# Performance work log

Measured on AMD Instinct MI355X. Metric: run time of the kernel, lower is better.

## Reference

```python
import jax, jax.numpy as jnp
import numpy as np

N = 100_000   # nodes
E = 1_600_000 # edges
F = 128       # node_feature_dim
H = 128       # hidden_dim
A = 32        # action_dim
G = 64        # graphs in batch


def setup_inputs() -> dict:
    key = jax.random.key(0)
    ks = jax.random.split(key, 12)
    s = 0.05
    return {
        "x": jax.random.normal(ks[0], (N, F), jnp.float32),
        "edge_index": jax.random.randint(ks[1], (2, E), 0, N, dtype=jnp.int32),
        "batch": jnp.sort(jax.random.randint(ks[2], (N,), 0, G, dtype=jnp.int32)),
        "W1": jax.random.normal(ks[3], (F, H), jnp.float32) * s,
        "b1": jnp.zeros((H,), jnp.float32),
        "W2": jax.random.normal(ks[4], (H, H), jnp.float32) * s,
        "b2": jnp.zeros((H,), jnp.float32),
        "Wa": jax.random.normal(ks[5], (H, A), jnp.float32) * s,
        "ba": jnp.zeros((A,), jnp.float32),
        "Wv": jax.random.normal(ks[6], (H, 1), jnp.float32) * s,
        "bv": jnp.zeros((1,), jnp.float32),
        "log_std": jnp.zeros((A,), jnp.float32),
    }


def reference(x, edge_index, batch, W1, b1, W2, b2, Wa, ba, Wv, bv, log_std):
    src, dst = edge_index[0], edge_index[1]
    # GCN symmetric norm with self-loops: deg_i = 1 + #incoming edges
    deg = jax.ops.segment_sum(jnp.ones((E,), x.dtype), dst, num_segments=N) + 1.0
    dinv = deg ** -0.5  # [N]

    def gcn(h, W, b):
        h = h @ W                                   # [N,H] dense transform first (as PyG GCNConv)
        msg = h[src] * dinv[src, None]              # gather + src norm
        agg = jax.ops.segment_sum(msg, dst, num_segments=N) * dinv[:, None]
        agg = agg + h * (dinv * dinv)[:, None]      # self-loop contribution
        return agg + b

    h = jax.nn.relu(gcn(x, W1, b1))
    h = jax.nn.relu(gcn(h, W2, b2))

    # global_mean_pool over graph segments
    counts = jax.ops.segment_sum(jnp.ones((N,), h.dtype), batch, num_segments=G)
    pooled = jax.ops.segment_sum(h, batch, num_segments=G) / jnp.maximum(counts, 1.0)[:, None]

    action_mean = pooled @ Wa + ba                  # [G,A]
    value = (pooled @ Wv + bv)[:, 0]                # [G]
    return action_mean, jnp.exp(log_std), value
```

## Files before the change

kernel.cpp:

```cpp
#include <hip/hip_runtime.h>
#include <hip/hip_bf16.h>

#define FDIM 128
#define HDIM 128
#define ADIM 32
#define PCH 128
#define BSH 6
#define BWD 64
#define CHUNK 8192
#define MAXNB 2048

#define CP(p) ((((p) & 7) << 4) | ((p) >> 3))

typedef short v8s __attribute__((ext_vector_type(8)));
typedef float v4f __attribute__((ext_vector_type(4)));
typedef float v2f __attribute__((ext_vector_type(2)));

static __device__ __forceinline__ float bflo(unsigned int u) {
    return __builtin_bit_cast(float, u << 16);
}
static __device__ __forceinline__ float bfhi(unsigned int u) {
    return __builtin_bit_cast(float, u & 0xffff0000u);
}
static __device__ __forceinline__ unsigned int bfpack(float a, float b) {
    unsigned int ua = __builtin_bit_cast(unsigned int, a);
    unsigned int ub = __builtin_bit_cast(unsigned int, b);
    ua += 0x7fffu + ((ua >> 16) & 1u);
    ub += 0x7fffu + ((ub >> 16) & 1u);
    return (ua >> 16) | (ub & 0xffff0000u);
}

#if defined(__has_builtin) && __has_builtin(__builtin_amdgcn_cvt_pk_f32_fp8) && \
    __has_builtin(__builtin_amdgcn_cvt_pk_fp8_f32)
#define FP8_HW 1
#endif

static __device__ __forceinline__ v2f fp8_dec_lo(unsigned int u) {
#ifdef FP8_HW
    return __builtin_amdgcn_cvt_pk_f32_fp8(u, false);
#else
    v2f r;
    #pragma unroll
    for (int i = 0; i < 2; ++i) {
        unsigned b = (u >> (8 * i)) & 0xffu;
        unsigned s = b >> 7, e = (b >> 3) & 0xfu, m = b & 7u;
        float v = (e == 0) ? (float)m * 0.001953125f
                           : __builtin_bit_cast(float, ((e + 120u) << 23) | (m << 20));
        r[i] = s ? -v : v;
    }
    return r;
#endif
}
static __device__ __forceinline__ v2f fp8_dec_hi(unsigned int u) {
#ifdef FP8_HW
    return __builtin_amdgcn_cvt_pk_f32_fp8(u, true);
#else
    return fp8_dec_lo(u >> 16);
#endif
}

#ifndef FP8_HW
static __device__ __forceinline__ unsigned int fp8_enc1(float x) {
    unsigned s = __builtin_bit_cast(unsigned, x) >> 31;
    float ax = fabsf(x);
    if (ax > 448.f) return (s << 7) | 0x7Eu;
    if (ax < 0.0009765625f) return s << 7;
    int e2 = (int)((__builtin_bit_cast(unsigned, ax) >> 23) & 0xff) - 127;
    int qe = (e2 < -6 ? -6 : e2) - 3;
    float q = __builtin_bit_cast(float, (unsigned)((qe + 127) << 23));
    float r = rintf(ax / q) * q;
    if (r > 448.f) return (s << 7) | 0x7Eu;
    if (r < 0.001953125f) return s << 7;
    unsigned ub = __builtin_bit_cast(unsigned, r);
    int re = (int)((ub >> 23) & 0xff) - 127;
    if (re < -6) {
        unsigned m = (unsigned)rintf(r * 512.f);
        return (s << 7) | m;
    }
    return (s << 7) | ((unsigned)(re + 7) << 3) | ((ub >> 20) & 7u);
}
#endif

static __device__ __forceinline__ unsigned int fp8x4_enc(float a, float b, float c, float d) {
#ifdef FP8_HW
    int p = __builtin_amdgcn_cvt_pk_fp8_f32(a, b, 0, false);
    p = __builtin_amdgcn_cvt_pk_fp8_f32(c, d, p, true);
    return (unsigned int)p;
#else
    return fp8_enc1(a) | (fp8_enc1(b) << 8) | (fp8_enc1(c) << 16) | (fp8_enc1(d) << 24);
#endif
}

__global__ __launch_bounds__(256) void block_hist_setup(const int* __restrict__ dst,
                                                        int* __restrict__ hist,
                                                        int E, int NB, int NBLK,
                                                        const float* __restrict__ W1,
                                                        const float* __restrict__ W2,
                                                        const float* __restrict__ b1,
                                                        const float* __restrict__ b2,
                                                        unsigned short* __restrict__ wsw1,
                                                        unsigned short* __restrict__ wsw2,
                                                        float* __restrict__ pb1,
                                                        float* __restrict__ pb2,
                                                        const int* __restrict__ batch,
                                                        int* __restrict__ gstart,
                                                        float* __restrict__ pooled,
                                                        int n, int G) {
    __shared__ int h[MAXNB];
    const int tid = threadIdx.x;
    if (blockIdx.x >= (unsigned)NBLK) {
        const int role = blockIdx.x - NBLK;
        if (role == 0) {
            for (int idx = tid; idx < 16384; idx += 256) {
                int nn = idx >> 7, k = idx & 127;
                wsw1[idx] = (unsigned short)(bfpack(W1[k * 128 + nn], 0.f) & 0xffffu);
                wsw2[idx] = (unsigned short)(bfpack(W2[CP(k) * 128 + nn], 0.f) & 0xffffu);
            }
            if (tid < 128) {
                pb1[tid] = b1[CP(tid)];
                pb2[tid] = b2[CP(tid)];
            }
        } else if (role == 1) {
            if (tid <= G) {
                int lo = 0, hi = n;
                while (lo < hi) { int mid = (lo + hi) >> 1; if (batch[mid] < tid) lo = mid + 1; else hi = mid; }
                gstart[tid] = lo;
            }
        } else {
            for (int i = tid; i < G * 128; i += 256) pooled[i] = 0.f;
        }
        return;
    }
    for (int i = tid; i < NB; i += 256) h[i] = 0;
    __syncthreads();
    const int base = blockIdx.x * CHUNK;
    int lim = base + CHUNK; if (lim > E) lim = E;
    for (int i = base + tid; i < lim; i += 256) atomicAdd(&h[dst[i] >> BSH], 1);
    __syncthreads();
    int* hrow = hist + (size_t)blockIdx.x * NB;
    for (int b = tid; b < NB; b += 256) hrow[b] = h[b];
}

__global__ void scanA(const int* __restrict__ hist, int* __restrict__ excl,
                      int* __restrict__ bsum, int M, int NB, int NBLK) {
    __shared__ int tmp[256];
    const int t = threadIdx.x;
    const int idx = blockIdx.x * 2048 + t * 8;
    int v[8], s = 0;
    #pragma unroll
    for (int i = 0; i < 8; ++i) {
        int p = idx + i;
        v[i] = (p < M) ? hist[(size_t)(p % NBLK) * NB + (p / NBLK)] : 0;
        s += v[i];
    }
    tmp[t] = s;
    __syncthreads();
    for (int off = 1; off < 256; off <<= 1) {
        int x = (t >= off) ? tmp[t - off] : 0;
        __syncthreads();
        tmp[t] += x;
        __syncthreads();
    }
    int run = tmp[t] - s;
    #pragma unroll
    for (int i = 0; i < 8; ++i) {
        int p = idx + i;
        if (p < M) excl[p] = run;
        run += v[i];
    }
    if (t == 255) bsum[blockIdx.x] = tmp[255];
}

__global__ void scanB(int* __restrict__ bsum, int nb) {
    __shared__ int tmp[256];
    const int t = threadIdx.x;
    int s = (t < nb) ? bsum[t] : 0;
    tmp[t] = s;
    __syncthreads();
    for (int off = 1; off < 256; off <<= 1) {
        int x = (t >= off) ? tmp[t - off] : 0;
        __syncthreads();
        tmp[t] += x;
        __syncthreads();
    }
    if (t < nb) bsum[t] = tmp[t] - s;
}

__global__ __launch_bounds__(256) void bucket_scatter(const int* __restrict__ src,
                                                      const int* __restrict__ dst,
                                                      const int* __restrict__ excl,
                                                      const int* __restrict__ bsum,
                                                      unsigned int* __restrict__ packed,
                                                      int E, int NB, int NBLK) {
    __shared__ int cur[MAXNB];
    const int tid = threadIdx.x;
    const int blk = blockIdx.x;
    for (int b = tid; b < NB; b += 256) {
        size_t p = (size_t)b * NBLK + blk;
        cur[b] = excl[p] + bsum[p >> 11];
    }
    __syncthreads();
    const int base = blk * CHUNK;
    int lim = base + CHUNK; if (lim > E) lim = E;
    for (int i = base + tid; i < lim; i += 256) {
        int d = dst[i];
        int s = src[i];
        int pos = atomicAdd(&cur[d >> BSH], 1);
        packed[pos] = (unsigned)s | ((unsigned)(d & (BWD - 1)) << 26);
    }
}

__global__ __launch_bounds__(256) void bucket_to_csr(const unsigned int* __restrict__ packed,
                                                     const int* __restrict__ excl,
                                                     const int* __restrict__ bsum,
                                                     int* __restrict__ rowptr,
                                                     float* __restrict__ dinv,
                                                     int* __restrict__ col,
                                                     int E, int N, int NB, int NBLK) {
    __shared__ int cnt[BWD];
    __shared__ int offs[BWD];
    const int b = blockIdx.x;
    const int tid = threadIdx.x;
    size_t p0 = (size_t)b * NBLK;
    const int base = excl[p0] + bsum[p0 >> 11];
    int next;
    if (b + 1 < NB) {
        size_t p1 = (size_t)(b + 1) * NBLK;
        next = excl[p1] + bsum[p1 >> 11];
    } else {
        next = E;
    }
    if (tid < BWD) cnt[tid] = 0;
    __syncthreads();
    for (int i = base + tid; i < next; i += 256) atomicAdd(&cnt[packed[i] >> 26], 1);
    __syncthreads();
    if (tid == 0) {
        int run = 0;
        for (int j = 0; j < BWD; ++j) { offs[j] = run; run += cnt[j]; }
    }
    __syncthreads();
    if (tid < BWD) {
        int node = (b << BSH) + tid;
        if (node < N) {
            rowptr[node] = base + offs[tid];
            dinv[node] = rsqrtf((float)cnt[tid] + 1.0f);
        }
        cnt[tid] = offs[tid];
    }
    if (b == NB - 1 && tid == 0) rowptr[N] = E;
    __syncthreads();
    for (int i = base + tid; i < next; i += 256) {
        unsigned int u = packed[i];
        int j = u >> 26;
        int pos = base + atomicAdd(&cnt[j], 1);
        col[pos] = (int)(u & 0x03ffffffu);
    }
}

template <bool BF16IN>
__global__ __launch_bounds__(256, 4) void gemm_mfma(const void* __restrict__ Xv,
                                                    const unsigned short* __restrict__ wsw,
                                                    const float* __restrict__ rowscale,
                                                    uint2* __restrict__ Out, int n) {
    const int tid = threadIdx.x;
    const int w = tid >> 6;
    const int lane = tid & 63;
    const int q = lane >> 4;
    const int m15 = lane & 15;
    const int rbase = blockIdx.x * 64;

    const int arow = rbase + w * 16 + m15;
    const int srow = (arow < n) ? arow : (n - 1);

    v8s a[4];
    if (BF16IN) {
        const unsigned short* xr = (const unsigned short*)Xv + (size_t)srow * 128 + q * 8;
        #pragma unroll
        for (int kk = 0; kk < 4; ++kk)
            a[kk] = __builtin_bit_cast(v8s, *(const uint4*)(xr + kk * 32));
    } else {
        const float* xr = (const float*)Xv + (size_t)srow * 128 + q * 8;
        #pragma unroll
        for (int kk = 0; kk < 4; ++kk) {
            float4 v0 = *(const float4*)(xr + kk * 32);
            float4 v1 = *(const float4*)(xr + kk * 32 + 4);
            uint4 p;
            p.x = bfpack(v0.x, v0.y); p.y = bfpack(v0.z, v0.w);
            p.z = bfpack(v1.x, v1.y); p.w = bfpack(v1.z, v1.w);
            a[kk] = __builtin_bit_cast(v8s, p);
        }
    }

    const v8s* __restrict__ pW = (const v8s*)wsw;
    v8s bcur[4], bnxt[4];
    #pragma unroll
    for (int kk = 0; kk < 4; ++kk) bcur[kk] = pW[(size_t)m15 * 16 + kk * 4 + q];

    v4f acc[8];
    #pragma unroll
    for (int nt = 0; nt < 8; ++nt) acc[nt] = (v4f){0.f, 0.f, 0.f, 0.f};

    #pragma unroll
    for (int nt = 0; nt < 8; ++nt) {
        if (nt < 7) {
            #pragma unroll
            for (int kk = 0; kk < 4; ++kk)
                bnxt[kk] = pW[(size_t)((nt + 1) * 16 + m15) * 16 + kk * 4 + q];
        }
        #pragma unroll
        for (int kk = 0; kk < 4; ++kk)
            acc[nt] = __builtin_amdgcn_mfma_f32_16x16x32_bf16(a[kk], bcur[kk], acc[nt], 0, 0, 0);
        #pragma unroll
        for (int kk = 0; kk < 4; ++kk) bcur[kk] = bnxt[kk];
    }

    #pragma unroll
    for (int reg = 0; reg < 4; ++reg) {
        int row = rbase + w * 16 + q * 4 + reg;
        if (row < n) {
            float sc = rowscale[row];
            unsigned int d0 = fp8x4_enc(acc[0][reg] * sc, acc[1][reg] * sc,
                                        acc[2][reg] * sc, acc[3][reg] * sc);
            unsigned int d1 = fp8x4_enc(acc[4][reg] * sc, acc[5][reg] * sc,
                                        acc[6][reg] * sc, acc[7][reg] * sc);
            Out[(size_t)row * 16 + m15] = make_uint2(d0, d1);
        }
    }
}

__global__ __launch_bounds__(256) void gather_fused(const unsigned int* __restrict__ T32,
                                                    const int* __restrict__ rowptr,
                                                    const int* __restrict__ col,
                                                    const float* __restrict__ dinv,
                                                    const float* __restrict__ pbias,
                                                    uint2* __restrict__ H, int n) {
    const int wave = (blockIdx.x * 256 + threadIdx.x) >> 6;
    const int d = wave * 2 + ((threadIdx.x >> 5) & 1);
    const int hl = threadIdx.x & 31;
    if (d >= n) return;
    int e = rowptr[d];
    const int end = rowptr[d + 1];

    v2f sl0 = {0.f, 0.f}, sh0 = {0.f, 0.f}, sl1 = {0.f, 0.f}, sh1 = {0.f, 0.f};

    if ((e & 1) && e < end) {
        unsigned int u = T32[(size_t)col[e] * 32 + hl];
        sl0 += fp8_dec_lo(u); sh0 += fp8_dec_hi(u);
        ++e;
    }
    for (; e + 7 < end; e += 8) {
        int2 p01 = *(const int2*)(col + e);
        int2 p23 = *(const int2*)(col + e + 2);
        int2 p45 = *(const int2*)(col + e + 4);
        int2 p67 = *(const int2*)(col + e + 6);
        unsigned int u0 = T32[(size_t)p01.x * 32 + hl];
        unsigned int u1 = T32[(size_t)p01.y * 32 + hl];
        unsigned int u2 = T32[(size_t)p23.x * 32 + hl];
        unsigned int u3 = T32[(size_t)p23.y * 32 + hl];
        unsigned int u4 = T32[(size_t)p45.x * 32 + hl];
        unsigned int u5 = T32[(size_t)p45.y * 32 + hl];
        unsigned int u6 = T32[(size_t)p67.x * 32 + hl];
        unsigned int u7 = T32[(size_t)p67.y * 32 + hl];
        sl0 += fp8_dec_lo(u0); sh0 += fp8_dec_hi(u0);
        sl1 += fp8_dec_lo(u1); sh1 += fp8_dec_hi(u1);
        sl0 += fp8_dec_lo(u2); sh0 += fp8_dec_hi(u2);
        sl1 += fp8_dec_lo(u3); sh1 += fp8_dec_hi(u3);
        sl0 += fp8_dec_lo(u4); sh0 += fp8_dec_hi(u4);
        sl1 += fp8_dec_lo(u5); sh1 += fp8_dec_hi(u5);
        sl0 += fp8_dec_lo(u6); sh0 += fp8_dec_hi(u6);
        sl1 += fp8_dec_lo(u7); sh1 += fp8_dec_hi(u7);
    }
    for (; e + 1 < end; e += 2) {
        int2 p = *(const int2*)(col + e);
        unsigned int u0 = T32[(size_t)p.x * 32 + hl];
        unsigned int u1 = T32[(size_t)p.y * 32 + hl];
        sl0 += fp8_dec_lo(u0); sh0 += fp8_dec_hi(u0);
        sl1 += fp8_dec_lo(u1); sh1 += fp8_dec_hi(u1);
    }
    if (e < end) {
        unsigned int u = T32[(size_t)col[e] * 32 + hl];
        sl0 += fp8_dec_lo(u); sh0 += fp8_dec_hi(u);
    }

    unsigned int su = T32[(size_t)d * 32 + hl];
    sl0 += fp8_dec_lo(su); sh0 += fp8_dec_hi(su);
    v2f sl = sl0 + sl1, sh = sh0 + sh1;

    const float di = dinv[d];
    const float4 bv = ((const float4*)pbias)[hl];
    float o0 = fmaxf(fmaf(sl.x, di, bv.x), 0.f);
    float o1 = fmaxf(fmaf(sl.y, di, bv.y), 0.f);
    float o2 = fmaxf(fmaf(sh.x, di, bv.z), 0.f);
    float o3 = fmaxf(fmaf(sh.y, di, bv.w), 0.f);
    uint2 o;
    o.x = bfpack(o0, o1);
    o.y = bfpack(o2, o3);
    H[(size_t)d * 32 + hl] = o;
}

__global__ __launch_bounds__(256) void pool_partial(const unsigned int* __restrict__ h2,
                                                    const int* __restrict__ batch,
                                                    float* __restrict__ pooled, int n) {
    const int c = threadIdx.x & 63;
    const int rl = threadIdx.x >> 6;
    int r = blockIdx.x * PCH + rl;
    int rend = blockIdx.x * PCH + PCH;
    if (rend > n) rend = n;
    v2f acc = {0.f, 0.f};
    int cur = -1;
    for (; r < rend; r += 4) {
        int g = batch[r];
        if (g != cur) {
            if (cur >= 0) {
                atomicAdd(&pooled[(size_t)cur * 128 + 2 * c], acc.x);
                atomicAdd(&pooled[(size_t)cur * 128 + 2 * c + 1], acc.y);
            }
            acc = (v2f){0.f, 0.f};
            cur = g;
        }
        unsigned int u = h2[(size_t)r * 64 + c];
        acc.x += bflo(u);
        acc.y += bfhi(u);
    }
    if (cur >= 0) {
        atomicAdd(&pooled[(size_t)cur * 128 + 2 * c], acc.x);
        atomicAdd(&pooled[(size_t)cur * 128 + 2 * c + 1], acc.y);
    }
}

__global__ void head_kernel(const float* __restrict__ pooled, const int* __restrict__ gstart,
                            const float* __restrict__ Wa, const float* __restrict__ ba,
                            const float* __restrict__ Wv, const float* __restrict__ bv,
                            const float* __restrict__ log_std, float* __restrict__ out, int G) {
    int g = blockIdx.x;
    int t = threadIdx.x;
    __shared__ float sp[128];
    float inv = 1.0f / fmaxf((float)(gstart[g + 1] - gstart[g]), 1.0f);
    sp[t] = pooled[(size_t)g * 128 + t] * inv;
    sp[t + 64] = pooled[(size_t)g * 128 + 64 + t] * inv;
    __syncthreads();
    if (t < 32) {
        float s = 0.f;
        #pragma unroll 8
        for (int k = 0; k < 128; ++k) s = fmaf(sp[k], Wa[CP(k) * ADIM + t], s);
        out[g * ADIM + t] = s + ba[t];
        if (g == 0) out[G * ADIM + t] = expf(log_std[t]);
    } else if (t == 32) {
        float s = 0.f;
        #pragma unroll 8
        for (int k = 0; k < 128; ++k) s = fmaf(sp[k], Wv[CP(k)], s);
        out[G * ADIM + ADIM + g] = s + bv[0];
    }
}

extern "C" void kernel_launch(void* const* d_in, const int* in_sizes, int n_in,
                              void* d_out, int out_size, void* d_ws, size_t ws_size,
                              hipStream_t stream) {
    const float* x       = (const float*)d_in[0];
    const int*   ei      = (const int*)d_in[1];
    const int*   batch   = (const int*)d_in[2];
    const float* W1      = (const float*)d_in[3];
    const float* b1      = (const float*)d_in[4];
    const float* W2      = (const float*)d_in[5];
    const float* b2      = (const float*)d_in[6];
    const float* Wa      = (const float*)d_in[7];
    const float* ba      = (const float*)d_in[8];
    const float* Wv      = (const float*)d_in[9];
    const float* bv      = (const float*)d_in[10];
    const float* log_std = (const float*)d_in[11];
    float* out = (float*)d_out;

    const int N = in_sizes[0] / FDIM;
    const int E = in_sizes[1] / 2;
    const int G = (out_size - ADIM) / (ADIM + 1);
    const int NB = (N + BWD - 1) >> BSH;
    const int NBLK = (E + CHUNK - 1) / CHUNK;
    const int M = NB * NBLK;
    const int nscanA = (M + 2047) / 2048;

    const int* src = ei;
    const int* dst = ei + E;

    auto align = [](size_t v) { return (v + 255) & ~(size_t)255; };
    char* ws = (char*)d_ws;
    size_t off = 0;
    int*   hist   = (int*)(ws + off);   off = align(off + (size_t)M * 4);
    int*   excl   = (int*)(ws + off);   off = align(off + (size_t)M * 4);
    int*   bsum   = (int*)(ws + off);   off = align(off + (size_t)256 * 4);
    int*   rowptr = (int*)(ws + off);   off = align(off + (size_t)(N + 1) * 4);
    int*   gstart = (int*)(ws + off);   off = align(off + (size_t)(G + 1) * 4);
    float* dinv   = (float*)(ws + off); off = align(off + (size_t)N * 4);
    float* pooled = (float*)(ws + off); off = align(off + (size_t)G * HDIM * 4);
    unsigned short* wsw1 = (unsigned short*)(ws + off); off = align(off + (size_t)16384 * 2);
    unsigned short* wsw2 = (unsigned short*)(ws + off); off = align(off + (size_t)16384 * 2);
    float* pb1    = (float*)(ws + off); off = align(off + (size_t)128 * 4);
    float* pb2    = (float*)(ws + off); off = align(off + (size_t)128 * 4);
    unsigned int* packed = (unsigned int*)(ws + off); off = align(off + (size_t)E * 4);
    int*   col    = (int*)(ws + off);   off = align(off + (size_t)E * 4);
    unsigned int* bufA = (unsigned int*)(ws + off); off = align(off + (size_t)N * 32 * 4);
    unsigned int* bufB = (unsigned int*)(ws + off); off = align(off + (size_t)N * 64 * 4);
    (void)ws_size;

    const int blkGemm = (N + 63) / 64;
    const int blkGather = (N + 7) / 8;
    const int blkPool = (N + PCH - 1) / PCH;

    block_hist_setup<<<NBLK + 3, 256, 0, stream>>>(dst, hist, E, NB, NBLK,
                                                   W1, W2, b1, b2, wsw1, wsw2, pb1, pb2,
                                                   batch, gstart, pooled, N, G);
    scanA<<<nscanA, 256, 0, stream>>>(hist, excl, bsum, M, NB, NBLK);
    scanB<<<1, 256, 0, stream>>>(bsum, nscanA);
    bucket_scatter<<<NBLK, 256, 0, stream>>>(src, dst, excl, bsum, packed, E, NB, NBLK);
    bucket_to_csr<<<NB, 256, 0, stream>>>(packed, excl, bsum, rowptr, dinv, col, E, N, NB, NBLK);

    gemm_mfma<false><<<blkGemm, 256, 0, stream>>>(x, wsw1, dinv, (uint2*)bufA, N);
    gather_fused<<<blkGather, 256, 0, stream>>>(bufA, rowptr, col, dinv, pb1,
                                                (uint2*)bufB, N);

    gemm_mfma<true><<<blkGemm, 256, 0, stream>>>(bufB, wsw2, dinv, (uint2*)bufA, N);
    gather_fused<<<blkGather, 256, 0, stream>>>(bufA, rowptr, col, dinv, pb2,
                                                (uint2*)bufB, N);

    pool_partial<<<blkPool, 256, 0, stream>>>(bufB, batch, pooled, N);
    head_kernel<<<G, 64, 0, stream>>>(pooled, gstart, Wa, ba, Wv, bv, log_std, out, G);
}
```

Baseline: 327.6 us.

## Fuse mean-pool into second gather and batch neighbour loads via shuffled column indices

The second GCN gather now accumulates pooled sums directly through shared-memory atomics, with a global-atomic fallback, instead of writing H and running a separate pool kernel. The gather loop is also restructured: each half-wave loads up to 32 column indices at once, broadcasts them by shuffle, and issues all row loads before decoding. Indices past the degree point at a zeroed padding row so the unrolled loads stay branch-free. This removes a kernel launch and the bf16 round-trip of the final features, and raises memory-level parallelism. In exchange it adds more registers per thread and more atomic traffic.

Result: slower. 360.3 us (+10.0%).

```diff
diff --git a/kernel.cpp b/kernel.cpp
--- a/kernel.cpp
+++ b/kernel.cpp
@@ -4,7 +4,6 @@
 #define FDIM 128
 #define HDIM 128
 #define ADIM 32
-#define PCH 128
 #define BSH 6
 #define BWD 64
 #define CHUNK 8192
@@ -105,6 +104,7 @@
                                                         const int* __restrict__ batch,
                                                         int* __restrict__ gstart,
                                                         float* __restrict__ pooled,
+                                                        unsigned int* __restrict__ zrow,
                                                         int n, int G) {
     __shared__ int h[MAXNB];
     const int tid = threadIdx.x;
@@ -128,6 +128,7 @@
             }
         } else {
             for (int i = tid; i < G * 128; i += 256) pooled[i] = 0.f;
+            if (tid < 32) zrow[tid] = 0u;
         }
         return;
     }
@@ -328,103 +329,114 @@
     }
 }
 
+template <int POOL>
 __global__ __launch_bounds__(256) void gather_fused(const unsigned int* __restrict__ T32,
                                                     const int* __restrict__ rowptr,
                                                     const int* __restrict__ col,
                                                     const float* __restrict__ dinv,
                                                     const float* __restrict__ pbias,
-                                                    uint2* __restrict__ H, int n) {
-    const int wave = (blockIdx.x * 256 + threadIdx.x) >> 6;
-    const int d = wave * 2 + ((threadIdx.x >> 5) & 1);
-    const int hl = threadIdx.x & 31;
-    if (d >= n) return;
-    int e = rowptr[d];
-    const int end = rowptr[d + 1];
-
-    v2f sl0 = {0.f, 0.f}, sh0 = {0.f, 0.f}, sl1 = {0.f, 0.f}, sh1 = {0.f, 0.f};
-
-    if ((e & 1) && e < end) {
-        unsigned int u = T32[(size_t)col[e] * 32 + hl];
-        sl0 += fp8_dec_lo(u); sh0 += fp8_dec_hi(u);
-        ++e;
-    }
-    for (; e + 7 < end; e += 8) {
-        int2 p01 = *(const int2*)(col + e);
-        int2 p23 = *(const int2*)(col + e + 2);
-        int2 p45 = *(const int2*)(col + e + 4);
-        int2 p67 = *(const int2*)(col + e + 6);
-        unsigned int u0 = T32[(size_t)p01.x * 32 + hl];
-        unsigned int u1 = T32[(size_t)p01.y * 32 + hl];
-        unsigned int u2 = T32[(size_t)p23.x * 32 + hl];
-        unsigned int u3 = T32[(size_t)p23.y * 32 + hl];
-        unsigned int u4 = T32[(size_t)p45.x * 32 + hl];
-        unsigned int u5 = T32[(size_t)p45.y * 32 + hl];
-        unsigned int u6 = T32[(size_t)p67.x * 32 + hl];
-        unsigned int u7 = T32[(size_t)p67.y * 32 + hl];
-        sl0 += fp8_dec_lo(u0); sh0 += fp8_dec_hi(u0);
-        sl1 += fp8_dec_lo(u1); sh1 += fp8_dec_hi(u1);
-        sl0 += fp8_dec_lo(u2); sh0 += fp8_dec_hi(u2);
-        sl1 += fp8_dec_lo(u3); sh1 += fp8_dec_hi(u3);
-        sl0 += fp8_dec_lo(u4); sh0 += fp8_dec_hi(u4);
-        sl1 += fp8_dec_lo(u5); sh1 += fp8_dec_hi(u5);
-        sl0 += fp8_dec_lo(u6); sh0 += fp8_dec_hi(u6);
-        sl1 += fp8_dec_lo(u7); sh1 += fp8_dec_hi(u7);
-    }
-    for (; e + 1 < end; e += 2) {
-        int2 p = *(const int2*)(col + e);
-        unsigned int u0 = T32[(size_t)p.x * 32 + hl];
-        unsigned int u1 = T32[(size_t)p.y * 32 + hl];
-        sl0 += fp8_dec_lo(u0); sh0 += fp8_dec_hi(u0);
-        sl1 += fp8_dec_lo(u1); sh1 += fp8_dec_hi(u1);
-    }
-    if (e < end) {
-        unsigned int u = T32[(size_t)col[e] * 32 + hl];
-        sl0 += fp8_dec_lo(u); sh0 += fp8_dec_hi(u);
-    }
-
-    unsigned int su = T32[(size_t)d * 32 + hl];
-    sl0 += fp8_dec_lo(su); sh0 += fp8_dec_hi(su);
-    v2f sl = sl0 + sl1, sh = sh0 + sh1;
-
-    const float di = dinv[d];
+                                                    uint2* __restrict__ H,
+                                                    float* __restrict__ pooled,
+                                                    const int* __restrict__ batch,
+                                                    int n, int nzrow) {
+    const int tid = threadIdx.x;
+    const int wave = (blockIdx.x * 256 + tid) >> 6;
+    const int d = wave * 2 + ((tid >> 5) & 1);
+    const int hl = tid & 31;
+    const bool act = d < n;
+
+    __shared__ float pacc[256];
+    int g0v = 0;
+    if (POOL) {
+        pacc[tid] = 0.f;
+        int d0 = blockIdx.x * 8;
+        g0v = batch[d0 < n ? d0 : (n - 1)];
+        __syncthreads();
+    }
+
+    int e0 = 0, deg = 0;
+    if (act) {
+        e0 = rowptr[d];
+        deg = rowptr[d + 1] - e0;
+    }
+    const int dc = act ? d : 0;
+    unsigned int su = T32[(size_t)dc * 32 + hl];
+
+    int cme = col[e0 + hl];
+
+    unsigned int u[32];
+    #pragma unroll
+    for (int b = 0; b < 4; ++b) {
+        if (deg > b * 8) {
+            #pragma unroll
+            for (int j = b * 8; j < b * 8 + 8; ++j) {
+                int cj = __shfl(cme, j, 32);
+                int cc = (j < deg) ? cj : nzrow;
+                u[j] = T32[(size_t)cc * 32 + hl];
+            }
+        }
+    }
+
+    v2f a0 = {0.f, 0.f}, a1 = {0.f, 0.f}, a2 = {0.f, 0.f}, a3 = {0.f, 0.f};
+    a0 += fp8_dec_lo(su);
+    a1 += fp8_dec_hi(su);
+
+    int degD = deg;
+    asm("" : "+v"(degD));
+    #pragma unroll
+    for (int b = 0; b < 4; ++b) {
+        if (degD > b * 8) {
+            #pragma unroll
+            for (int j = b * 8; j < b * 8 + 8; j += 2) {
+                a0 += fp8_dec_lo(u[j]);     a1 += fp8_dec_hi(u[j]);
+                a2 += fp8_dec_lo(u[j + 1]); a3 += fp8_dec_hi(u[j + 1]);
+            }
+        }
+    }
+
+    if (deg > 32) {
+        for (int e = e0 + 32; e < e0 + deg; ++e) {
+            unsigned int uu = T32[(size_t)col[e] * 32 + hl];
+            a0 += fp8_dec_lo(uu);
+            a1 += fp8_dec_hi(uu);
+        }
+    }
+
+    v2f sl = a0 + a2, sh = a1 + a3;
+    const float di = act ? dinv[d] : 0.f;
     const float4 bv = ((const float4*)pbias)[hl];
     float o0 = fmaxf(fmaf(sl.x, di, bv.x), 0.f);
     float o1 = fmaxf(fmaf(sl.y, di, bv.y), 0.f);
     float o2 = fmaxf(fmaf(sh.x, di, bv.z), 0.f);
     float o3 = fmaxf(fmaf(sh.y, di, bv.w), 0.f);
-    uint2 o;
-    o.x = bfpack(o0, o1);
-    o.y = bfpack(o2, o3);
-    H[(size_t)d * 32 + hl] = o;
-}
-
-__global__ __launch_bounds__(256) void pool_partial(const unsigned int* __restrict__ h2,
-                                                    const int* __restrict__ batch,
-                                                    float* __restrict__ pooled, int n) {
-    const int c = threadIdx.x & 63;
-    const int rl = threadIdx.x >> 6;
-    int r = blockIdx.x * PCH + rl;
-    int rend = blockIdx.x * PCH + PCH;
-    if (rend > n) rend = n;
-    v2f acc = {0.f, 0.f};
-    int cur = -1;
-    for (; r < rend; r += 4) {
-        int g = batch[r];
-        if (g != cur) {
-            if (cur >= 0) {
-                atomicAdd(&pooled[(size_t)cur * 128 + 2 * c], acc.x);
-                atomicAdd(&pooled[(size_t)cur * 128 + 2 * c + 1], acc.y);
+
+    if (POOL) {
+        if (act) {
+            int g = batch[d];
+            int gi = g - g0v;
+            if (gi < 2) {
+                atomicAdd(&pacc[gi * 128 + 4 * hl + 0], o0);
+                atomicAdd(&pacc[gi * 128 + 4 * hl + 1], o1);
+                atomicAdd(&pacc[gi * 128 + 4 * hl + 2], o2);
+                atomicAdd(&pacc[gi * 128 + 4 * hl + 3], o3);
+            } else {
+                atomicAdd(&pooled[(size_t)g * 128 + 4 * hl + 0], o0);
+                atomicAdd(&pooled[(size_t)g * 128 + 4 * hl + 1], o1);
+                atomicAdd(&pooled[(size_t)g * 128 + 4 * hl + 2], o2);
+                atomicAdd(&pooled[(size_t)g * 128 + 4 * hl + 3], o3);
             }
-            acc = (v2f){0.f, 0.f};
-            cur = g;
-        }
-        unsigned int u = h2[(size_t)r * 64 + c];
-        acc.x += bflo(u);
-        acc.y += bfhi(u);
-    }
-    if (cur >= 0) {
-        atomicAdd(&pooled[(size_t)cur * 128 + 2 * c], acc.x);
-        atomicAdd(&pooled[(size_t)cur * 128 + 2 * c + 1], acc.y);
+        }
+        __syncthreads();
+        float v = pacc[tid];
+        if (v != 0.f) {
+            int gg = g0v + (tid >> 7);
+            atomicAdd(&pooled[(size_t)gg * 128 + (tid & 127)], v);
+        }
+    } else if (act) {
+        uint2 o;
+        o.x = bfpack(o0, o1);
+        o.y = bfpack(o2, o3);
+        H[(size_t)d * 32 + hl] = o;
     }
 }
 
@@ -496,31 +508,31 @@
     float* pb1    = (float*)(ws + off); off = align(off + (size_t)128 * 4);
     float* pb2    = (float*)(ws + off); off = align(off + (size_t)128 * 4);
     unsigned int* packed = (unsigned int*)(ws + off); off = align(off + (size_t)E * 4);
-    int*   col    = (int*)(ws + off);   off = align(off + (size_t)E * 4);
-    unsigned int* bufA = (unsigned int*)(ws + off); off = align(off + (size_t)N * 32 * 4);
+    int*   col    = (int*)(ws + off);   off = align(off + (size_t)(E + 64) * 4);
+    unsigned int* bufA = (unsigned int*)(ws + off); off = align(off + (size_t)(N + 1) * 32 * 4);
     unsigned int* bufB = (unsigned int*)(ws + off); off = align(off + (size_t)N * 64 * 4);
     (void)ws_size;
 
+    unsigned int* zrow = bufA + (size_t)N * 32;
+
     const int blkGemm = (N + 63) / 64;
     const int blkGather = (N + 7) / 8;
-    const int blkPool = (N + PCH - 1) / PCH;
 
     block_hist_setup<<<NBLK + 3, 256, 0, stream>>>(dst, hist, E, NB, NBLK,
                                                    W1, W2, b1, b2, wsw1, wsw2, pb1, pb2,
-                                                   batch, gstart, pooled, N, G);
+                                                   batch, gstart, pooled, zrow, N, G);
     scanA<<<nscanA, 256, 0, stream>>>(hist, excl, bsum, M, NB, NBLK);
     scanB<<<1, 256, 0, stream>>>(bsum, nscanA);
     bucket_scatter<<<NBLK, 256, 0, stream>>>(src, dst, excl, bsum, packed, E, NB, NBLK);
     bucket_to_csr<<<NB, 256, 0, stream>>>(packed, excl, bsum, rowptr, dinv, col, E, N, NB, NBLK);
 
     gemm_mfma<false><<<blkGemm, 256, 0, stream>>>(x, wsw1, dinv, (uint2*)bufA, N);
-    gather_fused<<<blkGather, 256, 0, stream>>>(bufA, rowptr, col, dinv, pb1,
-                                                (uint2*)bufB, N);
+    gather_fused<0><<<blkGather, 256, 0, stream>>>(bufA, rowptr, col, dinv, pb1,
+                                                   (uint2*)bufB, nullptr, nullptr, N, N);
 
     gemm_mfma<true><<<blkGemm, 256, 0, stream>>>(bufB, wsw2, dinv, (uint2*)bufA, N);
-    gather_fused<<<blkGather, 256, 0, stream>>>(bufA, rowptr, col, dinv, pb2,
-                                                (uint2*)bufB, N);
-
-    pool_partial<<<blkPool, 256, 0, stream>>>(bufB, batch, pooled, N);
+    gather_fused<1><<<blkGather, 256, 0, stream>>>(bufA, rowptr, col, dinv, pb2,
+                                                   (uint2*)bufB, pooled, batch, N, N);
+
     head_kernel<<<G, 64, 0, stream>>>(pooled, gstart, Wa, ba, Wv, bv, log_std, out, G);
 }
```

## Pad CSR rows to multiples of eight with zero-row sentinel entries

Applied to the files above, without the earlier changes.

Builds the CSR with each node's neighbor list padded to a multiple of 8, using a dummy column index N that points at a zeroed extra row appended to the feature buffer. Each bucket gets a fixed-capacity region, and a per-node padded degree replaces rowptr[d+1]. The gather loop can then run entirely in its 8-wide unrolled path without scalar remainder iterations. The cost is extra loads of the zero row, a larger col array, and a fallback to unpadded layout when a bucket overflows its capacity.

After: 316.4 us. 1.04x faster.

```diff
diff --git a/kernel.cpp b/kernel.cpp
--- a/kernel.cpp
+++ b/kernel.cpp
@@ -9,6 +9,7 @@
 #define BWD 64
 #define CHUNK 8192
 #define MAXNB 2048
+#define CSRCAP 2048
 
 #define CP(p) ((((p) & 7) << 4) | ((p) >> 3))
 
@@ -105,6 +106,7 @@
                                                         const int* __restrict__ batch,
                                                         int* __restrict__ gstart,
                                                         float* __restrict__ pooled,
+                                                        unsigned int* __restrict__ zrow,
                                                         int n, int G) {
     __shared__ int h[MAXNB];
     const int tid = threadIdx.x;
@@ -128,6 +130,7 @@
             }
         } else {
             for (int i = tid; i < G * 128; i += 256) pooled[i] = 0.f;
+            if (tid < 32) zrow[tid] = 0u;
         }
         return;
     }
@@ -214,11 +217,13 @@
                                                      const int* __restrict__ excl,
                                                      const int* __restrict__ bsum,
                                                      int* __restrict__ rowptr,
+                                                     int* __restrict__ pdeg,
                                                      float* __restrict__ dinv,
                                                      int* __restrict__ col,
                                                      int E, int N, int NB, int NBLK) {
     __shared__ int cnt[BWD];
     __shared__ int offs[BWD];
+    __shared__ int ovf;
     const int b = blockIdx.x;
     const int tid = threadIdx.x;
     size_t p0 = (size_t)b * NBLK;
@@ -231,28 +236,39 @@
         next = E;
     }
     if (tid < BWD) cnt[tid] = 0;
+    if (tid == 0) ovf = 0;
     __syncthreads();
     for (int i = base + tid; i < next; i += 256) atomicAdd(&cnt[packed[i] >> 26], 1);
     __syncthreads();
+    const int rc = (tid < BWD) ? cnt[tid] : 0;
     if (tid == 0) {
         int run = 0;
-        for (int j = 0; j < BWD; ++j) { offs[j] = run; run += cnt[j]; }
-    }
-    __syncthreads();
+        for (int j = 0; j < BWD; ++j) { offs[j] = run; run += (cnt[j] + 7) & ~7; }
+        if (run > CSRCAP) {
+            ovf = 1;
+            run = 0;
+            for (int j = 0; j < BWD; ++j) { offs[j] = run; run += cnt[j]; }
+        }
+    }
+    __syncthreads();
+    const int cbase = b * CSRCAP;
     if (tid < BWD) {
         int node = (b << BSH) + tid;
         if (node < N) {
-            rowptr[node] = base + offs[tid];
-            dinv[node] = rsqrtf((float)cnt[tid] + 1.0f);
+            int pd = ovf ? rc : ((rc + 7) & ~7);
+            int st = cbase + offs[tid];
+            rowptr[node] = st;
+            pdeg[node] = pd;
+            dinv[node] = rsqrtf((float)rc + 1.0f);
+            for (int k = rc; k < pd; ++k) col[st + k] = N;
         }
         cnt[tid] = offs[tid];
     }
-    if (b == NB - 1 && tid == 0) rowptr[N] = E;
     __syncthreads();
     for (int i = base + tid; i < next; i += 256) {
         unsigned int u = packed[i];
         int j = u >> 26;
-        int pos = base + atomicAdd(&cnt[j], 1);
+        int pos = cbase + atomicAdd(&cnt[j], 1);
         col[pos] = (int)(u & 0x03ffffffu);
     }
 }
@@ -330,6 +346,7 @@
 
 __global__ __launch_bounds__(256) void gather_fused(const unsigned int* __restrict__ T32,
                                                     const int* __restrict__ rowptr,
+                                                    const int* __restrict__ pdeg,
                                                     const int* __restrict__ col,
                                                     const float* __restrict__ dinv,
                                                     const float* __restrict__ pbias,
@@ -339,7 +356,7 @@
     const int hl = threadIdx.x & 31;
     if (d >= n) return;
     int e = rowptr[d];
-    const int end = rowptr[d + 1];
+    const int end = e + pdeg[d];
 
     v2f sl0 = {0.f, 0.f}, sh0 = {0.f, 0.f}, sl1 = {0.f, 0.f}, sh1 = {0.f, 0.f};
 
@@ -488,6 +505,7 @@
     int*   excl   = (int*)(ws + off);   off = align(off + (size_t)M * 4);
     int*   bsum   = (int*)(ws + off);   off = align(off + (size_t)256 * 4);
     int*   rowptr = (int*)(ws + off);   off = align(off + (size_t)(N + 1) * 4);
+    int*   pdeg   = (int*)(ws + off);   off = align(off + (size_t)N * 4);
     int*   gstart = (int*)(ws + off);   off = align(off + (size_t)(G + 1) * 4);
     float* dinv   = (float*)(ws + off); off = align(off + (size_t)N * 4);
     float* pooled = (float*)(ws + off); off = align(off + (size_t)G * HDIM * 4);
@@ -496,10 +514,12 @@
     float* pb1    = (float*)(ws + off); off = align(off + (size_t)128 * 4);
     float* pb2    = (float*)(ws + off); off = align(off + (size_t)128 * 4);
     unsigned int* packed = (unsigned int*)(ws + off); off = align(off + (size_t)E * 4);
-    int*   col    = (int*)(ws + off);   off = align(off + (size_t)E * 4);
-    unsigned int* bufA = (unsigned int*)(ws + off); off = align(off + (size_t)N * 32 * 4);
+    int*   col    = (int*)(ws + off);   off = align(off + (size_t)NB * CSRCAP * 4);
+    unsigned int* bufA = (unsigned int*)(ws + off); off = align(off + (size_t)(N + 1) * 32 * 4);
     unsigned int* bufB = (unsigned int*)(ws + off); off = align(off + (size_t)N * 64 * 4);
     (void)ws_size;
+
+    unsigned int* zrow = bufA + (size_t)N * 32;
 
     const int blkGemm = (N + 63) / 64;
     const int blkGather = (N + 7) / 8;
@@ -507,18 +527,18 @@
 
     block_hist_setup<<<NBLK + 3, 256, 0, stream>>>(dst, hist, E, NB, NBLK,
                                                    W1, W2, b1, b2, wsw1, wsw2, pb1, pb2,
-                                                   batch, gstart, pooled, N, G);
+                                                   batch, gstart, pooled, zrow, N, G);
     scanA<<<nscanA, 256, 0, stream>>>(hist, excl, bsum, M, NB, NBLK);
     scanB<<<1, 256, 0, stream>>>(bsum, nscanA);
     bucket_scatter<<<NBLK, 256, 0, stream>>>(src, dst, excl, bsum, packed, E, NB, NBLK);
-    bucket_to_csr<<<NB, 256, 0, stream>>>(packed, excl, bsum, rowptr, dinv, col, E, N, NB, NBLK);
+    bucket_to_csr<<<NB, 256, 0, stream>>>(packed, excl, bsum, rowptr, pdeg, dinv, col, E, N, NB, NBLK);
 
     gemm_mfma<false><<<blkGemm, 256, 0, stream>>>(x, wsw1, dinv, (uint2*)bufA, N);
-    gather_fused<<<blkGather, 256, 0, stream>>>(bufA, rowptr, col, dinv, pb1,
+    gather_fused<<<blkGather, 256, 0, stream>>>(bufA, rowptr, pdeg, col, dinv, pb1,
                                                 (uint2*)bufB, N);
 
     gemm_mfma<true><<<blkGemm, 256, 0, stream>>>(bufB, wsw2, dinv, (uint2*)bufA, N);
-    gather_fused<<<blkGather, 256, 0, stream>>>(bufA, rowptr, col, dinv, pb2,
+    gather_fused<<<blkGather, 256, 0, stream>>>(bufA, rowptr, pdeg, col, dinv, pb2,
                                                 (uint2*)bufB, N);
 
     pool_partial<<<blkPool, 256, 0, stream>>>(bufB, batch, pooled, N);
```
